# Kernel tuning notes

Measured on AMD Instinct MI355X. Metric: run time of the kernel, lower is better.

The kernel has to match this reference:

```python
import jax, jax.numpy as jnp
import numpy as np

B, T, S = 32, 64, 128
ENC_H, DEC_H, ATTN, EMB = 512, 512, 256, 256
VOCAB, PAD = 32000, 0


def setup_inputs() -> dict:
    key = jax.random.key(0)
    ks = jax.random.split(key, 12)
    emb = jax.random.normal(ks[0], (VOCAB, EMB), jnp.float32) * 0.02
    emb = emb.at[PAD].set(0.0)  # padding_idx row zeroed
    in_dim = EMB + ENC_H
    return {
        "y_decoder_input": jax.random.randint(ks[1], (B, T), 0, VOCAB, jnp.int32),
        "encoder_outputs": jax.random.normal(ks[2], (B, S, ENC_H), jnp.float32),
        "decoder_init": jax.random.normal(ks[3], (1, B, DEC_H), jnp.float32),
        "encoder_mask": jnp.ones((B, S), jnp.int32),
        "embedding": emb,
        "W_enc": jax.random.normal(ks[4], (ENC_H, ATTN), jnp.float32) * 0.02,
        "W_dec": jax.random.normal(ks[5], (DEC_H, ATTN), jnp.float32) * 0.02,
        "v": jax.random.normal(ks[6], (ATTN,), jnp.float32) * 0.02,
        "W_ih": jax.random.normal(ks[7], (3 * DEC_H, in_dim), jnp.float32) * 0.02,
        "W_hh": jax.random.normal(ks[8], (3 * DEC_H, DEC_H), jnp.float32) * 0.02,
        "b_ih": jnp.zeros((3 * DEC_H,), jnp.float32),
        "b_hh": jnp.zeros((3 * DEC_H,), jnp.float32),
        "W_fc": jax.random.normal(ks[9], (DEC_H, VOCAB - 1), jnp.float32) * 0.02,
        "b_fc": jnp.zeros((VOCAB - 1,), jnp.float32),
    }


def reference(y_decoder_input, encoder_outputs, decoder_init, encoder_mask,
              embedding, W_enc, W_dec, v, W_ih, W_hh, b_ih, b_hh, W_fc, b_fc):
    H = decoder_init.shape[-1]
    embedded = embedding[y_decoder_input]            # [B,T,E]
    enc_proj = encoder_outputs @ W_enc               # [B,S,A] hoisted out of loop
    mask0 = encoder_mask == 0                        # [B,S]

    def step(h, emb_t):
        prev = h[-1]                                 # [B,H]
        # additive attention
        dec = prev @ W_dec                           # [B,A]
        energy = jnp.tanh(enc_proj + dec[:, None, :]) @ v   # [B,S]
        energy = jnp.where(mask0, -1e9, energy)
        aw = jax.nn.softmax(energy, axis=1)          # [B,S]
        context = jnp.einsum('bs,bsd->bd', aw, encoder_outputs)
        x = jnp.concatenate([emb_t, context], axis=1)  # [B, E+ENC_H]
        # GRU cell (PyTorch gate order r, z, n)
        gx = x @ W_ih.T + b_ih                       # [B,3H]
        gh = prev @ W_hh.T + b_hh                    # [B,3H]
        xr, xz, xn = gx[:, :H], gx[:, H:2*H], gx[:, 2*H:]
        hr, hz, hn = gh[:, :H], gh[:, H:2*H], gh[:, 2*H:]
        r = jax.nn.sigmoid(xr + hr)
        z = jax.nn.sigmoid(xz + hz)
        n = jnp.tanh(xn + r * hn)
        h_new = (1.0 - z) * n + z * prev
        out = h_new @ W_fc + b_fc                    # [B,V-1]
        return h_new[None], (out, aw)

    _, (outs, aws) = jax.lax.scan(step, decoder_init, jnp.swapaxes(embedded, 0, 1))
    outputs = jnp.swapaxes(outs, 0, 1)               # [B,T,V-1]
    attn_weights = jnp.swapaxes(aws, 0, 1)           # [B,T,S]
    return outputs, attn_weights
```

## Files before the change

kernel.cpp:

```cpp
#include <hip/hip_runtime.h>
#include <hip/hip_bf16.h>
#include <hip/hip_cooperative_groups.h>
#include <cstdint>
#include <cstddef>

#define B_   32
#define T_   64
#define S_   128
#define EH   512
#define DH   512
#define ATT  256
#define EMBD 256
#define V_   32000
#define VO   31999
#define G3   1536

#define ATTN_OFF 65533952

typedef __attribute__((ext_vector_type(8))) short bf16x8;
typedef __attribute__((ext_vector_type(4))) float f32x4;

static __device__ __forceinline__ unsigned short f2bf(float f) {
    union { float f; unsigned u; } x; x.f = f;
    unsigned r = (x.u + 0x7fffu + ((x.u >> 16) & 1u)) >> 16;
    return (unsigned short)r;
}

static __device__ __forceinline__ float fast_tanh(float x) {
    float xc = fminf(fmaxf(x, -15.0f), 15.0f);
    float e = __expf(2.0f * xc);
    return (e - 1.0f) / (e + 1.0f);
}

static __device__ __forceinline__ float fast_sig(float x) {
    return 1.0f / (1.0f + __expf(-x));
}

static __device__ __forceinline__ bf16x8 ldfrag(const unsigned long long* p) {
    union { unsigned long long u[2]; bf16x8 v; } x;
    x.u[0] = __hip_atomic_load(p,     __ATOMIC_RELAXED, __HIP_MEMORY_SCOPE_AGENT);
    x.u[1] = __hip_atomic_load(p + 1, __ATOMIC_RELAXED, __HIP_MEMORY_SCOPE_AGENT);
    return x.v;
}

static __device__ __forceinline__ void gbar(unsigned* cnt, unsigned* gen,
                                            unsigned target) {
    __syncthreads();
    if (threadIdx.x == 0) {
        unsigned old = __hip_atomic_fetch_add(cnt, 1u, __ATOMIC_RELEASE,
                                              __HIP_MEMORY_SCOPE_AGENT);
        if (old == 31u) {
            __hip_atomic_store(cnt, 0u, __ATOMIC_RELAXED, __HIP_MEMORY_SCOPE_AGENT);
            __hip_atomic_store(gen, target, __ATOMIC_RELEASE, __HIP_MEMORY_SCOPE_AGENT);
        } else {
            while (__hip_atomic_load(gen, __ATOMIC_RELAXED,
                                     __HIP_MEMORY_SCOPE_AGENT) != target) {}
        }
    }
    __syncthreads();
}

__global__ void k_trans_512x256(const float* __restrict__ in, float* __restrict__ out) {
    __shared__ float tile[32][33];
    int c0 = blockIdx.x * 32;
    int r0 = blockIdx.y * 32;
    int tx = threadIdx.x, ty = threadIdx.y;
#pragma unroll
    for (int q = 0; q < 4; q++)
        tile[ty + q*8][tx] = in[(r0 + ty + q*8) * 256 + c0 + tx];
    __syncthreads();
#pragma unroll
    for (int q = 0; q < 4; q++)
        out[(c0 + ty + q*8) * 512 + r0 + tx] = tile[tx][ty + q*8];
}

__global__ void k_wfc(const float* __restrict__ wfc, unsigned short* __restrict__ outT) {
    __shared__ float tile[32][33];
    int n0 = blockIdx.x * 32;
    int k0 = blockIdx.y * 32;
    int tx = threadIdx.x, ty = threadIdx.y;
#pragma unroll
    for (int q = 0; q < 4; q++) {
        int k = k0 + ty + q*8;
        int n = n0 + tx;
        tile[ty + q*8][tx] = (n < VO) ? wfc[(size_t)k * VO + n] : 0.0f;
    }
    __syncthreads();
#pragma unroll
    for (int q = 0; q < 4; q++) {
        int n = n0 + ty + q*8;
        int k = k0 + tx;
        outT[(size_t)n * 512 + k] = f2bf(tile[tx][ty + q*8]);
    }
}

__global__ void k_wpack(const float* __restrict__ W_ih, const float* __restrict__ W_hh,
                        unsigned short* __restrict__ Wp) {
    int idx = blockIdx.x * 256 + threadIdx.x;
    int e    = idx & 7;
    int lane = (idx >> 3) & 63;
    int q    = (idx >> 9) & 3;
    int kc   = (idx >> 11) & 31;
    int j    = idx >> 16;
    int io = lane & 15, ko = lane >> 4;
    int i = j * 16 + io;
    int k = kc * 32 + ko * 8 + e;
    int n = (q == 0) ? i : (q == 1) ? (512 + i) : (1024 + i);
    float val;
    if (k < 512) {
        val = (q == 3) ? 0.0f : W_ih[(size_t)n * 768 + 256 + k];
    } else {
        val = (q == 2) ? 0.0f : W_hh[(size_t)n * 512 + (k - 512)];
    }
    Wp[idx] = f2bf(val);
}

__global__ void k_hinit2(const float* __restrict__ di, float* __restrict__ h32,
                         unsigned short* __restrict__ Xf0, unsigned* __restrict__ bar) {
    int idx = blockIdx.x * 256 + threadIdx.x;
    float val = di[idx];
    h32[idx] = val;
    int b = idx >> 9, i = idx & 511;
    int mt = b >> 4, io = b & 15;
    int kc = 16 + (i >> 5), ko = (i >> 3) & 3, e = i & 7;
    Xf0[((((mt * 32 + kc) * 64) + ko * 16 + io) << 3) + e] = f2bf(val);
    if (idx == 0) { bar[0] = 0u; bar[1] = 0u; }
}

__global__ __launch_bounds__(256) void k_encproj(const float* __restrict__ enc,
                                                 const float* __restrict__ WencT,
                                                 float* __restrict__ ep) {
    int row0 = blockIdx.x * 16;
    int n = threadIdx.x;
    const float* wr = WencT + (size_t)n * 512;
    float acc[16];
#pragma unroll
    for (int r = 0; r < 16; r++) acc[r] = 0.0f;
    for (int k = 0; k < 512; k += 4) {
        float4 w = *(const float4*)(wr + k);
#pragma unroll
        for (int r = 0; r < 16; r++) {
            float4 x = *(const float4*)(enc + (size_t)(row0 + r) * 512 + k);
            acc[r] += x.x * w.x + x.y * w.y + x.z * w.z + x.w * w.w;
        }
    }
#pragma unroll
    for (int r = 0; r < 16; r++)
        ep[(size_t)(row0 + r) * 256 + n] = acc[r];
}

__global__ __launch_bounds__(256) void k_gxemb(const int* __restrict__ y,
                                               const float* __restrict__ embt,
                                               const float* __restrict__ W_ih,
                                               const float* __restrict__ bih,
                                               float* __restrict__ gx) {
    int row0 = blockIdx.y * 16;
    int col = blockIdx.x * 256 + threadIdx.x;
    const float* wr = W_ih + (size_t)col * 768;
    float acc[16];
#pragma unroll
    for (int r = 0; r < 16; r++) acc[r] = 0.0f;
    for (int k = 0; k < 256; k += 4) {
        float4 w = *(const float4*)(wr + k);
#pragma unroll
        for (int r = 0; r < 16; r++) {
            const float* xr = embt + (size_t)y[row0 + r] * 256 + k;
            float4 x = *(const float4*)xr;
            acc[r] += x.x * w.x + x.y * w.y + x.z * w.z + x.w * w.w;
        }
    }
    float bv = bih[col];
#pragma unroll
    for (int r = 0; r < 16; r++)
        gx[(size_t)(row0 + r) * G3 + col] = acc[r] + bv;
}

__global__ __launch_bounds__(512) void k_recur(
        const float* __restrict__ WdecT, const float* __restrict__ ep,
        const float* __restrict__ v, const int* __restrict__ mask,
        const float* __restrict__ enc, float* __restrict__ attn_out,
        const unsigned short* __restrict__ Wp, const float* __restrict__ gx_emb,
        const float* __restrict__ b_hh, const float* __restrict__ dinit,
        unsigned short* __restrict__ Xf0, unsigned short* __restrict__ Xf1,
        float* __restrict__ h32, unsigned short* __restrict__ Hall,
        unsigned* __restrict__ bar) {
    __shared__ uint4 Wlds4[6144];
    __shared__ float hbuf[512];
    __shared__ float decp[512];
    __shared__ float es[128];
    __shared__ float red[2];
    __shared__ float vs[256];
    __shared__ int   msk[128];
    __shared__ float bhs[48];
    __shared__ float hloc[512];
    __shared__ float pacc[2048];
    __shared__ unsigned g0s;

    int bid = blockIdx.x, tid = threadIdx.x;
    int b = bid;
    int j = bid;
    int w = tid >> 6, lane = tid & 63;

    char* WldsB = (char*)Wlds4;
    unsigned* bcnt = bar;
    unsigned* bgen = bar + 1;

    for (int it = 0; it < 12; it++) {
        int cid = it * 512 + tid;
        int c = cid >> 6, off = cid & 63;
        int q, kc;
        if (c < 32)      { q = 0; kc = c; }
        else if (c < 64) { q = 1; kc = c - 32; }
        else if (c < 80) { q = 2; kc = c - 64; }
        else             { q = 3; kc = c - 80 + 16; }
        const uint4* src = (const uint4*)Wp + ((size_t)((j * 32 + kc) * 4 + q) << 6) + off;
        Wlds4[c * 64 + off] = *src;
    }
    if (tid < 256) vs[tid] = v[tid];
    if (tid < 128) msk[tid] = mask[b * 128 + tid];
    if (tid < 48)  bhs[tid] = b_hh[(tid >> 4) * 512 + j * 16 + (tid & 15)];
    hloc[tid] = dinit[(size_t)(tid >> 4) * 512 + j * 16 + (tid & 15)];
    if (tid == 0)
        g0s = __hip_atomic_load(bgen, __ATOMIC_RELAXED, __HIP_MEMORY_SCOPE_AGENT);
    __syncthreads();
    unsigned bt = g0s;

    const float* epb  = ep  + (size_t)b * 128 * 256;
    const float* encb = enc + (size_t)b * 128 * 512;

    for (int t = 0; t < T_; t++) {
        unsigned short* Xcur = (t & 1) ? Xf1 : Xf0;
        unsigned short* Xnxt = (t & 1) ? Xf0 : Xf1;

        hbuf[tid] = __hip_atomic_load(&h32[b * 512 + tid], __ATOMIC_RELAXED,
                                      __HIP_MEMORY_SCOPE_AGENT);
        __syncthreads();
        {
            int d = tid & 255, half = tid >> 8;
            const float* wr = WdecT + (size_t)d * 512 + half * 256;
            const float* hb = hbuf + half * 256;
            float acc = 0.0f;
#pragma unroll 8
            for (int k = 0; k < 256; k += 4) {
                float4 wv = *(const float4*)(wr + k);
                float4 xv = *(const float4*)(hb + k);
                acc += xv.x * wv.x + xv.y * wv.y + xv.z * wv.z + xv.w * wv.w;
            }
            decp[tid] = acc;
        }
        __syncthreads();
        if (tid < 256) decp[tid] += decp[tid + 256];
        __syncthreads();
        {
            float d0 = decp[lane], d1 = decp[lane + 64],
                  d2 = decp[lane + 128], d3 = decp[lane + 192];
            float v0 = vs[lane], v1 = vs[lane + 64],
                  v2 = vs[lane + 128], v3 = vs[lane + 192];
#pragma unroll
            for (int si = 0; si < 16; si++) {
                int s = w * 16 + si;
                const float* er = epb + (size_t)s * 256;
                float e = fast_tanh(er[lane] + d0) * v0
                        + fast_tanh(er[lane + 64] + d1) * v1
                        + fast_tanh(er[lane + 128] + d2) * v2
                        + fast_tanh(er[lane + 192] + d3) * v3;
#pragma unroll
                for (int o = 32; o; o >>= 1) e += __shfl_xor(e, o);
                if (lane == 0)
                    es[s] = (msk[s] == 0) ? -1e9f : e;
            }
        }
        __syncthreads();
        if (tid < 64) {
            float a = fmaxf(es[tid], es[tid + 64]);
#pragma unroll
            for (int o = 32; o; o >>= 1) a = fmaxf(a, __shfl_xor(a, o));
            if (tid == 0) red[0] = a;
        }
        __syncthreads();
        float mx = red[0];
        if (tid < 128) es[tid] = __expf(es[tid] - mx);
        __syncthreads();
        if (tid < 64) {
            float a = es[tid] + es[tid + 64];
#pragma unroll
            for (int o = 32; o; o >>= 1) a += __shfl_xor(a, o);
            if (tid == 0) red[1] = a;
        }
        __syncthreads();
        float inv = 1.0f / red[1];
        if (tid < 128) {
            float aw = es[tid] * inv;
            es[tid] = aw;
            attn_out[(size_t)b * (T_ * S_) + t * S_ + tid] = aw;
        }
        __syncthreads();
        {
            float a1 = 0.0f;
            const float* eb = encb + tid;
#pragma unroll 8
            for (int s = 0; s < 128; s++)
                a1 += es[s] * eb[(size_t)s * 512];
            int d = tid;
            unsigned short mybf = f2bf(a1);
            int oth = __shfl_down((int)mybf, 1);
            int hw = (((b >> 4) * 32 + (d >> 5)) * 64 + ((d >> 3) & 3) * 16 + (b & 15)) * 8 + (d & 7);
            if (!(d & 1)) {
                unsigned pk = ((unsigned)mybf & 0xffffu) | ((unsigned)oth << 16);
                __hip_atomic_store((unsigned*)Xcur + (hw >> 1), pk,
                                   __ATOMIC_RELAXED, __HIP_MEMORY_SCOPE_AGENT);
            }
        }
        gbar(bcnt, bgen, ++bt);

        float ge_r, ge_z, ge_n;
        int gb = tid >> 4, gi = j * 16 + (tid & 15);
        {
            const float* g = gx_emb + (size_t)(gb * 64 + t) * G3;
            ge_r = g[gi]; ge_z = g[512 + gi]; ge_n = g[1024 + gi];
        }
        if (w < 6) {
            int mt = w & 1, g = w >> 1;
            const unsigned long long* Xg8 = (const unsigned long long*)Xcur;
            f32x4 acc0 = {0.f, 0.f, 0.f, 0.f};
            f32x4 acc1 = {0.f, 0.f, 0.f, 0.f};
            if (g < 2) {
                const char* wb = WldsB + (g ? 32768 : 0);
#pragma unroll
                for (int kc = 0; kc < 32; kc++) {
                    bf16x8 av = ldfrag(Xg8 + (size_t)((mt * 32 + kc) * 64 + lane) * 2);
                    bf16x8 bv = *(const bf16x8*)(wb + kc * 1024 + lane * 16);
                    acc0 = __builtin_amdgcn_mfma_f32_16x16x32_bf16(av, bv, acc0, 0, 0, 0);
                }
            } else {
#pragma unroll
                for (int kc = 0; kc < 16; kc++) {
                    bf16x8 av = ldfrag(Xg8 + (size_t)((mt * 32 + kc) * 64 + lane) * 2);
                    bf16x8 bv = *(const bf16x8*)(WldsB + 65536 + kc * 1024 + lane * 16);
                    acc0 = __builtin_amdgcn_mfma_f32_16x16x32_bf16(av, bv, acc0, 0, 0, 0);
                }
#pragma unroll
                for (int kc = 16; kc < 32; kc++) {
                    bf16x8 av = ldfrag(Xg8 + (size_t)((mt * 32 + kc) * 64 + lane) * 2);
                    bf16x8 bv = *(const bf16x8*)(WldsB + 81920 + (kc - 16) * 1024 + lane * 16);
                    acc1 = __builtin_amdgcn_mfma_f32_16x16x32_bf16(av, bv, acc1, 0, 0, 0);
                }
            }
            int row = lane >> 4, col = lane & 15;
            if (g < 2) {
#pragma unroll
                for (int reg = 0; reg < 4; reg++)
                    pacc[((g * 2 + mt) * 16 + row * 4 + reg) * 16 + col] = acc0[reg];
            } else {
#pragma unroll
                for (int reg = 0; reg < 4; reg++)
                    pacc[((2 * 2 + mt) * 16 + row * 4 + reg) * 16 + col] = acc0[reg];
#pragma unroll
                for (int reg = 0; reg < 4; reg++)
                    pacc[((3 * 2 + mt) * 16 + row * 4 + reg) * 16 + col] = acc1[reg];
            }
        }
        __syncthreads();
        {
            int i2 = tid & 15;
            int mt = gb >> 4, rrow = gb & 15;
            float rp = pacc[((0 * 2 + mt) * 16 + rrow) * 16 + i2];
            float zp = pacc[((1 * 2 + mt) * 16 + rrow) * 16 + i2];
            float nx = pacc[((2 * 2 + mt) * 16 + rrow) * 16 + i2];
            float nh = pacc[((3 * 2 + mt) * 16 + rrow) * 16 + i2];
            float r = fast_sig(ge_r + rp + bhs[i2]);
            float z = fast_sig(ge_z + zp + bhs[16 + i2]);
            float n = fast_tanh(ge_n + nx + r * (nh + bhs[32 + i2]));
            float prev = hloc[tid];
            float hv = (1.0f - z) * n + z * prev;
            hloc[tid] = hv;
            __hip_atomic_store(&h32[gb * 512 + gi], hv, __ATOMIC_RELAXED,
                               __HIP_MEMORY_SCOPE_AGENT);
            unsigned short hb16 = f2bf(hv);
            int oth = __shfl_down((int)hb16, 1);
            int i = gi;
            int hw = ((mt * 32 + 16 + (i >> 5)) * 64 + ((i >> 3) & 3) * 16 + rrow) * 8 + (i & 7);
            if (!(tid & 1)) {
                unsigned pk = ((unsigned)hb16 & 0xffffu) | ((unsigned)oth << 16);
                __hip_atomic_store((unsigned*)Xnxt + (hw >> 1), pk,
                                   __ATOMIC_RELAXED, __HIP_MEMORY_SCOPE_AGENT);
            }
            Hall[(size_t)(gb * 64 + t) * 512 + i] = hb16;
        }
        gbar(bcnt, bgen, ++bt);
    }
}

__global__ __launch_bounds__(256) void k_fc(const unsigned short* __restrict__ A,
                                            const unsigned short* __restrict__ Bt,
                                            const float* __restrict__ bias,
                                            float* __restrict__ out) {
    __shared__ char smem[65536];
    unsigned short* Abuf = (unsigned short*)smem;
    unsigned short* Bbuf = (unsigned short*)(smem + 10240);
    int tid = threadIdx.x;
    int n0 = blockIdx.x * 128, m0 = blockIdx.y * 128;
    int w = tid >> 6, lane = tid & 63;
    int wm = w >> 1, wn = w & 1;
    int io = lane & 15, ko = lane >> 4;

    const uint4* Ag = (const uint4*)A;
    const uint4* Bg = (const uint4*)Bt;

    f32x4 z4 = {0.f, 0.f, 0.f, 0.f};
    f32x4 acc[4][4];
#pragma unroll
    for (int a = 0; a < 4; a++)
#pragma unroll
        for (int b = 0; b < 4; b++) acc[a][b] = z4;

    for (int k0 = 0; k0 < 512; k0 += 32) {
        uint4 av[2], bv[2];
#pragma unroll
        for (int u = 0; u < 2; u++) {
            int c = tid + u * 256;
            int r = c >> 2, ch = c & 3;
            av[u] = Ag[(size_t)(m0 + r) * 64 + (k0 >> 3) + ch];
            bv[u] = Bg[(size_t)(n0 + r) * 64 + (k0 >> 3) + ch];
        }
        __syncthreads();
#pragma unroll
        for (int u = 0; u < 2; u++) {
            int c = tid + u * 256;
            int r = c >> 2, ch = c & 3;
            *(uint4*)((char*)Abuf + r * 80 + ch * 16) = av[u];
            *(uint4*)((char*)Bbuf + r * 80 + ch * 16) = bv[u];
        }
        __syncthreads();
        bf16x8 af[4], bf[4];
#pragma unroll
        for (int s = 0; s < 4; s++) {
            af[s] = *(const bf16x8*)((char*)Abuf + (wm * 64 + s * 16 + io) * 80 + ko * 16);
            bf[s] = *(const bf16x8*)((char*)Bbuf + (wn * 64 + s * 16 + io) * 80 + ko * 16);
        }
#pragma unroll
        for (int sm = 0; sm < 4; sm++)
#pragma unroll
            for (int sn = 0; sn < 4; sn++)
                acc[sm][sn] = __builtin_amdgcn_mfma_f32_16x16x32_bf16(af[sm], bf[sn], acc[sm][sn], 0, 0, 0);
    }

    __syncthreads();
    float* Cst = (float*)smem;
#pragma unroll
    for (int sm = 0; sm < 4; sm++)
#pragma unroll
        for (int sn = 0; sn < 4; sn++) {
            int cc = wn * 64 + sn * 16 + io;
#pragma unroll
            for (int reg = 0; reg < 4; reg++) {
                int rr = wm * 64 + sm * 16 + ko * 4 + reg;
                Cst[rr * 128 + cc] = acc[sm][sn][reg];
            }
        }
    __syncthreads();
    {
        int c = tid & 127, rh = tid >> 7;
        int ng = n0 + c;
        if (ng < VO) {
            float bv = bias[ng];
#pragma unroll 8
            for (int i = 0; i < 64; i++) {
                int r = i * 2 + rh;
                out[(size_t)(m0 + r) * VO + ng] = Cst[r * 128 + c] + bv;
            }
        }
    }
}

extern "C" void kernel_launch(void* const* d_in, const int* in_sizes, int n_in,
                              void* d_out, int out_size, void* d_ws, size_t ws_size,
                              hipStream_t stream) {
    const int*   y      = (const int*)d_in[0];
    const float* enc    = (const float*)d_in[1];
    const float* dinit  = (const float*)d_in[2];
    const int*   mask   = (const int*)d_in[3];
    const float* embt   = (const float*)d_in[4];
    const float* W_enc  = (const float*)d_in[5];
    const float* W_dec  = (const float*)d_in[6];
    const float* v      = (const float*)d_in[7];
    const float* W_ih   = (const float*)d_in[8];
    const float* W_hh   = (const float*)d_in[9];
    const float* b_ih   = (const float*)d_in[10];
    const float* b_hh   = (const float*)d_in[11];
    const float* W_fc   = (const float*)d_in[12];
    const float* b_fc   = (const float*)d_in[13];
    float* out = (float*)d_out;

    char* ws = (char*)d_ws;
    size_t o = 0;
    float* enc_proj = (float*)(ws + o);          o += (size_t)4096 * 256 * 4;
    float* gx_emb   = (float*)(ws + o);          o += (size_t)2048 * 1536 * 4;
    float* WencT    = (float*)(ws + o);          o += (size_t)256 * 512 * 4;
    float* WdecT    = (float*)(ws + o);          o += (size_t)256 * 512 * 4;
    unsigned short* Wp   = (unsigned short*)(ws + o); o += (size_t)2097152 * 2;
    unsigned short* WfcT = (unsigned short*)(ws + o); o += (size_t)32000 * 512 * 2;
    unsigned short* Hall = (unsigned short*)(ws + o); o += (size_t)2048 * 512 * 2;
    unsigned short* Xf0  = (unsigned short*)(ws + o); o += (size_t)32768 * 2;
    unsigned short* Xf1  = (unsigned short*)(ws + o); o += (size_t)32768 * 2;
    float* h32 = (float*)(ws + o);               o += (size_t)32 * 512 * 4;
    unsigned* bar = (unsigned*)(ws + o);         o += 256;

    k_trans_512x256<<<dim3(8, 16), dim3(32, 8), 0, stream>>>(W_enc, WencT);
    k_trans_512x256<<<dim3(8, 16), dim3(32, 8), 0, stream>>>(W_dec, WdecT);
    k_wfc<<<dim3(1000, 16), dim3(32, 8), 0, stream>>>(W_fc, WfcT);
    k_wpack<<<8192, 256, 0, stream>>>(W_ih, W_hh, Wp);
    k_hinit2<<<64, 256, 0, stream>>>(dinit, h32, Xf0, bar);
    k_encproj<<<256, 256, 0, stream>>>(enc, WencT, enc_proj);
    k_gxemb<<<dim3(6, 128), 256, 0, stream>>>(y, embt, W_ih, b_ih, gx_emb);

    float* attn_out = out + ATTN_OFF;

    {
        const float* WdecT_c = WdecT; const float* ep_c = enc_proj;
        const unsigned short* Wp_c = Wp; const float* gx_c = gx_emb;
        void* args[] = {
            (void*)&WdecT_c, (void*)&ep_c, (void*)&v, (void*)&mask,
            (void*)&enc, (void*)&attn_out, (void*)&Wp_c, (void*)&gx_c,
            (void*)&b_hh, (void*)&dinit, (void*)&Xf0, (void*)&Xf1,
            (void*)&h32, (void*)&Hall, (void*)&bar
        };
        hipLaunchCooperativeKernel((void*)k_recur, dim3(32), dim3(512),
                                   args, 0, stream);
    }

    k_fc<<<dim3(250, 16), 256, 0, stream>>>(Hall, WfcT, b_fc, out);
}
```

Baseline: 3.073 ms.

## Split recurrent kernel across 192 blocks with specialized attention and GRU roles

Expands the cooperative recurrent kernel from 32 to 192 blocks. Each batch row's attention is split across four blocks that combine partial energies through a per-batch counter, and each GRU column slice is split into two K-halves. The hidden-state half of the gate matmul runs during the attention phase, overlapping it with attention work, and is later merged through a global partial buffer. The goal is to use more CUs and shorten the per-step critical path. In exchange there are more blocks in every grid barrier, extra global-memory partial exchanges, and additional spin waits.

```diff
diff --git a/kernel.cpp b/kernel.cpp
--- a/kernel.cpp
+++ b/kernel.cpp
@@ -15,6 +15,10 @@
 #define VO   31999
 #define G3   1536
 
+#define NATT 128
+#define NGRU 64
+#define NBLK 192
+
 #define ATTN_OFF 65533952
 
 typedef __attribute__((ext_vector_type(8))) short bf16x8;
@@ -36,20 +40,13 @@
     return 1.0f / (1.0f + __expf(-x));
 }
 
-static __device__ __forceinline__ bf16x8 ldfrag(const unsigned long long* p) {
-    union { unsigned long long u[2]; bf16x8 v; } x;
-    x.u[0] = __hip_atomic_load(p,     __ATOMIC_RELAXED, __HIP_MEMORY_SCOPE_AGENT);
-    x.u[1] = __hip_atomic_load(p + 1, __ATOMIC_RELAXED, __HIP_MEMORY_SCOPE_AGENT);
-    return x.v;
-}
-
 static __device__ __forceinline__ void gbar(unsigned* cnt, unsigned* gen,
                                             unsigned target) {
     __syncthreads();
     if (threadIdx.x == 0) {
         unsigned old = __hip_atomic_fetch_add(cnt, 1u, __ATOMIC_RELEASE,
                                               __HIP_MEMORY_SCOPE_AGENT);
-        if (old == 31u) {
+        if (old == (unsigned)(NBLK - 1)) {
             __hip_atomic_store(cnt, 0u, __ATOMIC_RELAXED, __HIP_MEMORY_SCOPE_AGENT);
             __hip_atomic_store(gen, target, __ATOMIC_RELEASE, __HIP_MEMORY_SCOPE_AGENT);
         } else {
@@ -124,7 +121,7 @@
     int mt = b >> 4, io = b & 15;
     int kc = 16 + (i >> 5), ko = (i >> 3) & 3, e = i & 7;
     Xf0[((((mt * 32 + kc) * 64) + ko * 16 + io) << 3) + e] = f2bf(val);
-    if (idx == 0) { bar[0] = 0u; bar[1] = 0u; }
+    if (idx < 64) bar[idx] = 0u;
 }
 
 __global__ __launch_bounds__(256) void k_encproj(const float* __restrict__ enc,
@@ -183,43 +180,51 @@
         const float* __restrict__ b_hh, const float* __restrict__ dinit,
         unsigned short* __restrict__ Xf0, unsigned short* __restrict__ Xf1,
         float* __restrict__ h32, unsigned short* __restrict__ Hall,
-        unsigned* __restrict__ bar) {
-    __shared__ uint4 Wlds4[6144];
-    __shared__ float hbuf[512];
-    __shared__ float decp[512];
-    __shared__ float es[128];
-    __shared__ float red[2];
-    __shared__ float vs[256];
-    __shared__ int   msk[128];
-    __shared__ float bhs[48];
-    __shared__ float hloc[512];
-    __shared__ float pacc[2048];
+        unsigned* __restrict__ bar, float* __restrict__ epart,
+        float* __restrict__ gpart) {
+    __shared__ char smem[96512];
     __shared__ unsigned g0s;
 
     int bid = blockIdx.x, tid = threadIdx.x;
-    int b = bid;
-    int j = bid;
     int w = tid >> 6, lane = tid & 63;
-
-    char* WldsB = (char*)Wlds4;
     unsigned* bcnt = bar;
     unsigned* bgen = bar + 1;
-
-    for (int it = 0; it < 12; it++) {
-        int cid = it * 512 + tid;
-        int c = cid >> 6, off = cid & 63;
-        int q, kc;
-        if (c < 32)      { q = 0; kc = c; }
-        else if (c < 64) { q = 1; kc = c - 32; }
-        else if (c < 80) { q = 2; kc = c - 64; }
-        else             { q = 3; kc = c - 80 + 16; }
-        const uint4* src = (const uint4*)Wp + ((size_t)((j * 32 + kc) * 4 + q) << 6) + off;
-        Wlds4[c * 64 + off] = *src;
-    }
-    if (tid < 256) vs[tid] = v[tid];
-    if (tid < 128) msk[tid] = mask[b * 128 + tid];
-    if (tid < 48)  bhs[tid] = b_hh[(tid >> 4) * 512 + j * 16 + (tid & 15)];
-    hloc[tid] = dinit[(size_t)(tid >> 4) * 512 + j * 16 + (tid & 15)];
+    unsigned* ecnt = bar + 8;
+
+    const bool is_att = (bid < NATT);
+
+    float* hbuf = (float*)smem;
+    float* pdec = (float*)(smem + 2048);
+    float* decs = (float*)(smem + 4352);
+    float* es   = (float*)(smem + 4608);
+    float* redv = (float*)(smem + 5120);
+    float* vsl  = (float*)(smem + 5152);
+    int*   mskl = (int*)(smem + 5408);
+    float* pctx = (float*)(smem + 5920);
+    uint4* wg   = (uint4*)smem;
+    uint4* xst  = (uint4*)(smem + 49152);
+    float* pacc = (float*)(smem + 81920);
+    float* gprt = (float*)(smem + 88064);
+    float* hloc = (float*)(smem + 94208);
+    float* bhsl = (float*)(smem + 96256);
+
+    int b = 0, nu = 0, j = 0, kh = 0;
+    if (is_att) {
+        b = bid >> 2; nu = bid & 3;
+        if (tid < 64)  vsl[tid] = v[nu * 64 + tid];
+        if (tid < 128) mskl[tid] = mask[b * 128 + tid];
+    } else {
+        int g_ = bid - NATT; j = g_ >> 1; kh = g_ & 1;
+        for (int c = tid; c < 3072; c += 512) {
+            int gg = c >> 10, kcl = (c >> 6) & 15, ln = c & 63;
+            int q = (gg == 2) ? (kh ? 3 : 2) : gg;
+            int kc = kh * 16 + kcl;
+            wg[(gg * 16 + kcl) * 64 + ln] =
+                ((const uint4*)Wp)[(size_t)((j * 32 + kc) * 4 + q) * 64 + ln];
+        }
+        hloc[tid] = dinit[(size_t)(tid >> 4) * 512 + j * 16 + (tid & 15)];
+        if (tid < 48) bhsl[tid] = b_hh[(tid >> 4) * 512 + j * 16 + (tid & 15)];
+    }
     if (tid == 0)
         g0s = __hip_atomic_load(bgen, __ATOMIC_RELAXED, __HIP_MEMORY_SCOPE_AGENT);
     __syncthreads();
@@ -227,166 +232,224 @@
 
     const float* epb  = ep  + (size_t)b * 128 * 256;
     const float* encb = enc + (size_t)b * 128 * 512;
+    int mtb = b >> 4, iob = b & 15;
 
     for (int t = 0; t < T_; t++) {
         unsigned short* Xcur = (t & 1) ? Xf1 : Xf0;
         unsigned short* Xnxt = (t & 1) ? Xf0 : Xf1;
-
-        hbuf[tid] = __hip_atomic_load(&h32[b * 512 + tid], __ATOMIC_RELAXED,
-                                      __HIP_MEMORY_SCOPE_AGENT);
-        __syncthreads();
-        {
-            int d = tid & 255, half = tid >> 8;
-            const float* wr = WdecT + (size_t)d * 512 + half * 256;
-            const float* hb = hbuf + half * 256;
-            float acc = 0.0f;
+        float ge_r = 0.f, ge_z = 0.f, ge_n = 0.f;
+
+        if (is_att) {
+            hbuf[tid] = __hip_atomic_load(&h32[b * 512 + tid], __ATOMIC_RELAXED,
+                                          __HIP_MEMORY_SCOPE_AGENT);
+            __syncthreads();
+            {
+                const float* wr = WdecT + (size_t)(nu * 64 + lane) * 512 + w * 64;
+                const float* hb = hbuf + w * 64;
+                float acc = 0.f;
+#pragma unroll
+                for (int k = 0; k < 64; k += 4) {
+                    float4 wv = *(const float4*)(wr + k);
+                    acc += wv.x * hb[k] + wv.y * hb[k + 1]
+                         + wv.z * hb[k + 2] + wv.w * hb[k + 3];
+                }
+                pdec[lane * 9 + w] = acc;
+            }
+            __syncthreads();
+            if (tid < 64) {
+                float a = 0.f;
+#pragma unroll
+                for (int kp = 0; kp < 8; kp++) a += pdec[tid * 9 + kp];
+                decs[tid] = a;
+            }
+            __syncthreads();
+            {
+                float dq = decs[lane], vq = vsl[lane];
+#pragma unroll
+                for (int si = 0; si < 16; si++) {
+                    int s = w * 16 + si;
+                    float e = fast_tanh(epb[(size_t)s * 256 + nu * 64 + lane] + dq) * vq;
+#pragma unroll
+                    for (int o = 32; o; o >>= 1) e += __shfl_xor(e, o);
+                    if (lane == 0)
+                        __hip_atomic_store(&epart[((b << 2) + nu) * 128 + s], e,
+                                           __ATOMIC_RELAXED, __HIP_MEMORY_SCOPE_AGENT);
+                }
+            }
+            __syncthreads();
+            if (tid == 0) {
+                __hip_atomic_fetch_add(&ecnt[b], 1u, __ATOMIC_RELEASE,
+                                       __HIP_MEMORY_SCOPE_AGENT);
+                unsigned tgt = 4u * (unsigned)(t + 1);
+                while (__hip_atomic_load(&ecnt[b], __ATOMIC_RELAXED,
+                                         __HIP_MEMORY_SCOPE_AGENT) < tgt) {}
+            }
+            __syncthreads();
+            if (tid < 128) {
+                const float* epr = epart + (size_t)(b << 2) * 128 + tid;
+                float e = __hip_atomic_load(epr,       __ATOMIC_RELAXED, __HIP_MEMORY_SCOPE_AGENT)
+                        + __hip_atomic_load(epr + 128, __ATOMIC_RELAXED, __HIP_MEMORY_SCOPE_AGENT)
+                        + __hip_atomic_load(epr + 256, __ATOMIC_RELAXED, __HIP_MEMORY_SCOPE_AGENT)
+                        + __hip_atomic_load(epr + 384, __ATOMIC_RELAXED, __HIP_MEMORY_SCOPE_AGENT);
+                es[tid] = (mskl[tid] == 0) ? -1e9f : e;
+            }
+            __syncthreads();
+            if (tid < 64) {
+                float a = fmaxf(es[tid], es[tid + 64]);
+#pragma unroll
+                for (int o = 32; o; o >>= 1) a = fmaxf(a, __shfl_xor(a, o));
+                if (tid == 0) redv[0] = a;
+            }
+            __syncthreads();
+            float mx = redv[0];
+            if (tid < 128) es[tid] = __expf(es[tid] - mx);
+            __syncthreads();
+            if (tid < 64) {
+                float a = es[tid] + es[tid + 64];
+#pragma unroll
+                for (int o = 32; o; o >>= 1) a += __shfl_xor(a, o);
+                if (tid == 0) redv[1] = a;
+            }
+            __syncthreads();
+            float inv = 1.0f / redv[1];
+            if (tid < 128) {
+                float aw = es[tid] * inv;
+                es[tid] = aw;
+                if (nu == 0)
+                    attn_out[(size_t)b * (T_ * S_) + t * S_ + tid] = aw;
+            }
+            __syncthreads();
+            {
+                int d2 = tid & 127, sh = tid >> 7;
+                const float* eb = encb + nu * 128 + d2;
+                float a1 = 0.f;
 #pragma unroll 8
-            for (int k = 0; k < 256; k += 4) {
-                float4 wv = *(const float4*)(wr + k);
-                float4 xv = *(const float4*)(hb + k);
-                acc += xv.x * wv.x + xv.y * wv.y + xv.z * wv.z + xv.w * wv.w;
-            }
-            decp[tid] = acc;
-        }
-        __syncthreads();
-        if (tid < 256) decp[tid] += decp[tid + 256];
-        __syncthreads();
-        {
-            float d0 = decp[lane], d1 = decp[lane + 64],
-                  d2 = decp[lane + 128], d3 = decp[lane + 192];
-            float v0 = vs[lane], v1 = vs[lane + 64],
-                  v2 = vs[lane + 128], v3 = vs[lane + 192];
-#pragma unroll
-            for (int si = 0; si < 16; si++) {
-                int s = w * 16 + si;
-                const float* er = epb + (size_t)s * 256;
-                float e = fast_tanh(er[lane] + d0) * v0
-                        + fast_tanh(er[lane + 64] + d1) * v1
-                        + fast_tanh(er[lane + 128] + d2) * v2
-                        + fast_tanh(er[lane + 192] + d3) * v3;
-#pragma unroll
-                for (int o = 32; o; o >>= 1) e += __shfl_xor(e, o);
-                if (lane == 0)
-                    es[s] = (msk[s] == 0) ? -1e9f : e;
-            }
-        }
-        __syncthreads();
-        if (tid < 64) {
-            float a = fmaxf(es[tid], es[tid + 64]);
-#pragma unroll
-            for (int o = 32; o; o >>= 1) a = fmaxf(a, __shfl_xor(a, o));
-            if (tid == 0) red[0] = a;
-        }
-        __syncthreads();
-        float mx = red[0];
-        if (tid < 128) es[tid] = __expf(es[tid] - mx);
-        __syncthreads();
-        if (tid < 64) {
-            float a = es[tid] + es[tid + 64];
-#pragma unroll
-            for (int o = 32; o; o >>= 1) a += __shfl_xor(a, o);
-            if (tid == 0) red[1] = a;
-        }
-        __syncthreads();
-        float inv = 1.0f / red[1];
-        if (tid < 128) {
-            float aw = es[tid] * inv;
-            es[tid] = aw;
-            attn_out[(size_t)b * (T_ * S_) + t * S_ + tid] = aw;
-        }
-        __syncthreads();
-        {
-            float a1 = 0.0f;
-            const float* eb = encb + tid;
-#pragma unroll 8
-            for (int s = 0; s < 128; s++)
-                a1 += es[s] * eb[(size_t)s * 512];
-            int d = tid;
-            unsigned short mybf = f2bf(a1);
-            int oth = __shfl_down((int)mybf, 1);
-            int hw = (((b >> 4) * 32 + (d >> 5)) * 64 + ((d >> 3) & 3) * 16 + (b & 15)) * 8 + (d & 7);
-            if (!(d & 1)) {
-                unsigned pk = ((unsigned)mybf & 0xffffu) | ((unsigned)oth << 16);
-                __hip_atomic_store((unsigned*)Xcur + (hw >> 1), pk,
-                                   __ATOMIC_RELAXED, __HIP_MEMORY_SCOPE_AGENT);
-            }
-        }
-        gbar(bcnt, bgen, ++bt);
-
-        float ge_r, ge_z, ge_n;
-        int gb = tid >> 4, gi = j * 16 + (tid & 15);
-        {
+                for (int s = sh * 32; s < sh * 32 + 32; s++)
+                    a1 += es[s] * eb[(size_t)s * 512];
+                pctx[sh * 129 + d2] = a1;
+            }
+            __syncthreads();
+            if (tid < 128) {
+                float c = pctx[tid] + pctx[129 + tid] + pctx[258 + tid] + pctx[387 + tid];
+                unsigned short mybf = f2bf(c);
+                int oth = __shfl_down((int)mybf, 1);
+                int d = nu * 128 + tid;
+                int hw = ((mtb * 32 + (d >> 5)) * 64 + ((d >> 3) & 3) * 16 + iob) * 8 + (d & 7);
+                if (!(tid & 1)) {
+                    unsigned pk = ((unsigned)mybf & 0xffffu) | ((unsigned)oth << 16);
+                    __hip_atomic_store((unsigned*)Xcur + (hw >> 1), pk,
+                                       __ATOMIC_RELAXED, __HIP_MEMORY_SCOPE_AGENT);
+                }
+            }
+        } else if (kh == 1) {
+            const unsigned long long* Xg = (const unsigned long long*)Xcur;
+#pragma unroll
+            for (int u = 0; u < 8; u++) {
+                int lw = u * 512 + tid;
+                int mtl = lw >> 11, r = lw & 2047;
+                int kcl = r >> 7, rr = r & 127;
+                size_t gw = (size_t)((mtl * 32 + 16 + kcl) * 128) + rr;
+                ((unsigned long long*)xst)[lw] =
+                    __hip_atomic_load(Xg + gw, __ATOMIC_RELAXED, __HIP_MEMORY_SCOPE_AGENT);
+            }
+            __syncthreads();
+            if (w < 6) {
+                int mt = w & 1, gg = w >> 1;
+                f32x4 acc = {0.f, 0.f, 0.f, 0.f};
+                const uint4* xw  = xst + mt * 16 * 64;
+                const uint4* wgg = wg + gg * 16 * 64;
+#pragma unroll
+                for (int kcl = 0; kcl < 16; kcl++) {
+                    uint4 a  = xw[kcl * 64 + lane];
+                    uint4 bv = wgg[kcl * 64 + lane];
+                    acc = __builtin_amdgcn_mfma_f32_16x16x32_bf16(
+                        *(const bf16x8*)&a, *(const bf16x8*)&bv, acc, 0, 0, 0);
+                }
+                int row = lane >> 4, col = lane & 15;
+                float* gp = gpart + (size_t)j * 1536;
+#pragma unroll
+                for (int reg = 0; reg < 4; reg++)
+                    __hip_atomic_store(&gp[((gg * 2 + mt) * 16 + row * 4 + reg) * 16 + col],
+                                       acc[reg], __ATOMIC_RELAXED, __HIP_MEMORY_SCOPE_AGENT);
+            }
+        } else {
+            int gb = tid >> 4, gi = j * 16 + (tid & 15);
             const float* g = gx_emb + (size_t)(gb * 64 + t) * G3;
             ge_r = g[gi]; ge_z = g[512 + gi]; ge_n = g[1024 + gi];
         }
-        if (w < 6) {
-            int mt = w & 1, g = w >> 1;
-            const unsigned long long* Xg8 = (const unsigned long long*)Xcur;
-            f32x4 acc0 = {0.f, 0.f, 0.f, 0.f};
-            f32x4 acc1 = {0.f, 0.f, 0.f, 0.f};
-            if (g < 2) {
-                const char* wb = WldsB + (g ? 32768 : 0);
-#pragma unroll
-                for (int kc = 0; kc < 32; kc++) {
-                    bf16x8 av = ldfrag(Xg8 + (size_t)((mt * 32 + kc) * 64 + lane) * 2);
-                    bf16x8 bv = *(const bf16x8*)(wb + kc * 1024 + lane * 16);
-                    acc0 = __builtin_amdgcn_mfma_f32_16x16x32_bf16(av, bv, acc0, 0, 0, 0);
-                }
-            } else {
-#pragma unroll
-                for (int kc = 0; kc < 16; kc++) {
-                    bf16x8 av = ldfrag(Xg8 + (size_t)((mt * 32 + kc) * 64 + lane) * 2);
-                    bf16x8 bv = *(const bf16x8*)(WldsB + 65536 + kc * 1024 + lane * 16);
-                    acc0 = __builtin_amdgcn_mfma_f32_16x16x32_bf16(av, bv, acc0, 0, 0, 0);
-                }
-#pragma unroll
-                for (int kc = 16; kc < 32; kc++) {
-                    bf16x8 av = ldfrag(Xg8 + (size_t)((mt * 32 + kc) * 64 + lane) * 2);
-                    bf16x8 bv = *(const bf16x8*)(WldsB + 81920 + (kc - 16) * 1024 + lane * 16);
-                    acc1 = __builtin_amdgcn_mfma_f32_16x16x32_bf16(av, bv, acc1, 0, 0, 0);
-                }
-            }
-            int row = lane >> 4, col = lane & 15;
-            if (g < 2) {
+
+        gbar(bcnt, bgen, ++bt);
+
+        if (!is_att && kh == 0) {
+            const unsigned long long* Xg = (const unsigned long long*)Xcur;
+#pragma unroll
+            for (int u = 0; u < 8; u++) {
+                int lw = u * 512 + tid;
+                int mtl = lw >> 11, r = lw & 2047;
+                int kcl = r >> 7, rr = r & 127;
+                size_t gw = (size_t)((mtl * 32 + kcl) * 128) + rr;
+                ((unsigned long long*)xst)[lw] =
+                    __hip_atomic_load(Xg + gw, __ATOMIC_RELAXED, __HIP_MEMORY_SCOPE_AGENT);
+            }
+            __syncthreads();
+            if (w < 6) {
+                int mt = w & 1, gg = w >> 1;
+                f32x4 acc = {0.f, 0.f, 0.f, 0.f};
+                const uint4* xw  = xst + mt * 16 * 64;
+                const uint4* wgg = wg + gg * 16 * 64;
+#pragma unroll
+                for (int kcl = 0; kcl < 16; kcl++) {
+                    uint4 a  = xw[kcl * 64 + lane];
+                    uint4 bv = wgg[kcl * 64 + lane];
+                    acc = __builtin_amdgcn_mfma_f32_16x16x32_bf16(
+                        *(const bf16x8*)&a, *(const bf16x8*)&bv, acc, 0, 0, 0);
+                }
+                int row = lane >> 4, col = lane & 15;
 #pragma unroll
                 for (int reg = 0; reg < 4; reg++)
-                    pacc[((g * 2 + mt) * 16 + row * 4 + reg) * 16 + col] = acc0[reg];
-            } else {
-#pragma unroll
-                for (int reg = 0; reg < 4; reg++)
-                    pacc[((2 * 2 + mt) * 16 + row * 4 + reg) * 16 + col] = acc0[reg];
-#pragma unroll
-                for (int reg = 0; reg < 4; reg++)
-                    pacc[((3 * 2 + mt) * 16 + row * 4 + reg) * 16 + col] = acc1[reg];
-            }
-        }
-        __syncthreads();
-        {
-            int i2 = tid & 15;
-            int mt = gb >> 4, rrow = gb & 15;
-            float rp = pacc[((0 * 2 + mt) * 16 + rrow) * 16 + i2];
-            float zp = pacc[((1 * 2 + mt) * 16 + rrow) * 16 + i2];
-            float nx = pacc[((2 * 2 + mt) * 16 + rrow) * 16 + i2];
-            float nh = pacc[((3 * 2 + mt) * 16 + rrow) * 16 + i2];
-            float r = fast_sig(ge_r + rp + bhs[i2]);
-            float z = fast_sig(ge_z + zp + bhs[16 + i2]);
-            float n = fast_tanh(ge_n + nx + r * (nh + bhs[32 + i2]));
-            float prev = hloc[tid];
-            float hv = (1.0f - z) * n + z * prev;
-            hloc[tid] = hv;
-            __hip_atomic_store(&h32[gb * 512 + gi], hv, __ATOMIC_RELAXED,
-                               __HIP_MEMORY_SCOPE_AGENT);
-            unsigned short hb16 = f2bf(hv);
-            int oth = __shfl_down((int)hb16, 1);
-            int i = gi;
-            int hw = ((mt * 32 + 16 + (i >> 5)) * 64 + ((i >> 3) & 3) * 16 + rrow) * 8 + (i & 7);
-            if (!(tid & 1)) {
-                unsigned pk = ((unsigned)hb16 & 0xffffu) | ((unsigned)oth << 16);
-                __hip_atomic_store((unsigned*)Xnxt + (hw >> 1), pk,
-                                   __ATOMIC_RELAXED, __HIP_MEMORY_SCOPE_AGENT);
-            }
-            Hall[(size_t)(gb * 64 + t) * 512 + i] = hb16;
-        }
+                    pacc[((gg * 2 + mt) * 16 + row * 4 + reg) * 16 + col] = acc[reg];
+            }
+            {
+                const float* gp = gpart + (size_t)j * 1536;
+#pragma unroll
+                for (int u = 0; u < 3; u++) {
+                    int i5 = u * 512 + tid;
+                    gprt[i5] = __hip_atomic_load(&gp[i5], __ATOMIC_RELAXED,
+                                                 __HIP_MEMORY_SCOPE_AGENT);
+                }
+            }
+            __syncthreads();
+            {
+                int gb = tid >> 4, i2 = tid & 15;
+                int mt = gb >> 4, row = gb & 15;
+                int base0 = ((0 * 2 + mt) * 16 + row) * 16 + i2;
+                int base1 = ((1 * 2 + mt) * 16 + row) * 16 + i2;
+                int base2 = ((2 * 2 + mt) * 16 + row) * 16 + i2;
+                float rp = pacc[base0] + gprt[base0];
+                float zp = pacc[base1] + gprt[base1];
+                float nx = pacc[base2];
+                float nh = gprt[base2];
+                float r = fast_sig(ge_r + rp + bhsl[i2]);
+                float z = fast_sig(ge_z + zp + bhsl[16 + i2]);
+                float n = fast_tanh(ge_n + nx + r * (nh + bhsl[32 + i2]));
+                float prev = hloc[tid];
+                float hv = (1.0f - z) * n + z * prev;
+                hloc[tid] = hv;
+                int gi = j * 16 + i2;
+                __hip_atomic_store(&h32[gb * 512 + gi], hv, __ATOMIC_RELAXED,
+                                   __HIP_MEMORY_SCOPE_AGENT);
+                unsigned short hb16 = f2bf(hv);
+                int oth = __shfl_down((int)hb16, 1);
+                int hw = ((mt * 32 + 16 + (gi >> 5)) * 64 + ((gi >> 3) & 3) * 16 + row) * 8 + (gi & 7);
+                if (!(tid & 1)) {
+                    unsigned pk = ((unsigned)hb16 & 0xffffu) | ((unsigned)oth << 16);
+                    __hip_atomic_store((unsigned*)Xnxt + (hw >> 1), pk,
+                                       __ATOMIC_RELAXED, __HIP_MEMORY_SCOPE_AGENT);
+                }
+                Hall[(size_t)(gb * 64 + t) * 512 + gi] = hb16;
+            }
+        }
+
         gbar(bcnt, bgen, ++bt);
     }
 }
@@ -505,6 +568,8 @@
     unsigned short* Xf1  = (unsigned short*)(ws + o); o += (size_t)32768 * 2;
     float* h32 = (float*)(ws + o);               o += (size_t)32 * 512 * 4;
     unsigned* bar = (unsigned*)(ws + o);         o += 256;
+    float* epart = (float*)(ws + o);             o += (size_t)32 * 4 * 128 * 4;
+    float* gpart = (float*)(ws + o);             o += (size_t)32 * 1536 * 4;
 
     k_trans_512x256<<<dim3(8, 16), dim3(32, 8), 0, stream>>>(W_enc, WencT);
     k_trans_512x256<<<dim3(8, 16), dim3(32, 8), 0, stream>>>(W_dec, WdecT);
@@ -523,9 +588,10 @@
             (void*)&WdecT_c, (void*)&ep_c, (void*)&v, (void*)&mask,
             (void*)&enc, (void*)&attn_out, (void*)&Wp_c, (void*)&gx_c,
             (void*)&b_hh, (void*)&dinit, (void*)&Xf0, (void*)&Xf1,
-            (void*)&h32, (void*)&Hall, (void*)&bar
+            (void*)&h32, (void*)&Hall, (void*)&bar, (void*)&epart,
+            (void*)&gpart
         };
-        hipLaunchCooperativeKernel((void*)k_recur, dim3(32), dim3(512),
+        hipLaunchCooperativeKernel((void*)k_recur, dim3(NBLK), dim3(512),
                                    args, 0, stream);
     }
 
```

Result: slower. 3.468 ms (+12.9%).
